# Kernel optimization log

Hardware: AMD Instinct MI355X
Metric: run time of the kernel (lower is better)

The kernel has to match this reference:

```python
import jax, jax.numpy as jnp
import numpy as np
import math
from jax import lax

K = 3  # kernel size for every layer


def _get_size(h, w, stride, ceil_mode):
    ah, aw = h - (K - 1), w - (K - 1)
    if ceil_mode:
        return math.ceil(ah / stride), math.ceil(aw / stride)
    return ah // stride, aw // stride


def _sample(h, w, stride, ceil_mode, mask_out, rng):
    """Replicates SConv2dAvg.sample: random in-stride offsets per output cell,
    plus bottom-up input mask = union of 3x3 windows of selected positions
    where the downstream mask is active."""
    ah, aw = h - (K - 1), w - (K - 1)
    oh, ow = _get_size(h, w, stride, ceil_mode)
    selh = rng.integers(0, stride, (oh, ow)).astype(np.int32)
    selw = rng.integers(0, stride, (oh, ow)).astype(np.int32)
    resth, restw = oh * stride - ah, ow * stride - aw
    if resth > 0:
        selh[-1, :] = selh[-1, :] % resth
    if restw > 0:
        selw[:, -1] = selw[:, -1] % restw
    ph = selh + (np.arange(oh) * stride)[:, None]  # conv-grid row of selected window
    pw = selw + (np.arange(ow) * stride)[None, :]
    mask_in = np.zeros((h, w), np.int32)
    ys = ph[mask_out == 1]
    xs = pw[mask_out == 1]
    for dy in range(K):
        for dx in range(K):
            mask_in[ys + dy, xs + dx] = 1
    return selh, selw, mask_in


def setup_inputs() -> dict:
    key = jax.random.key(0)
    rng = np.random.default_rng(0)
    B, H0, W0 = 64, 132, 132
    ks = jax.random.split(key, 9)
    x = jax.random.normal(ks[0], (B, 3, H0, W0), jnp.float32)

    def conv_params(kw_, kb_, cout, cin):
        bound = 1.0 / np.sqrt(cin * K * K)
        w = jax.random.uniform(kw_, (cout, cin, K, K), jnp.float32, -bound, bound)
        b = jax.random.uniform(kb_, (cout,), jnp.float32, -bound, bound)
        return w, b

    w1, b1 = conv_params(ks[1], ks[2], 200, 3)
    w2, b2 = conv_params(ks[3], ks[4], 400, 200)
    w3, b3 = conv_params(ks[5], ks[6], 800, 400)
    w4, b4 = conv_params(ks[7], ks[8], 10, 800)

    h1, wd1 = _get_size(H0, W0, 2, False)   # 65,65
    h2, wd2 = _get_size(h1, wd1, 2, False)  # 31,31
    h3, wd3 = _get_size(h2, wd2, 2, True)   # 15,15
    mask3 = np.ones((h3, wd3), np.int32)
    selh3, selw3, mask2 = _sample(h2, wd2, 2, True, mask3, rng)
    selh2, selw2, mask1 = _sample(h1, wd1, 2, False, mask2, rng)
    selh1, selw1, _ = _sample(H0, W0, 2, False, mask1, rng)

    j = jnp.asarray
    return {
        "x": x,
        "w1": w1, "b1": b1, "w2": w2, "b2": b2,
        "w3": w3, "b3": b3, "w4": w4, "b4": b4,
        "selh1": j(selh1), "selw1": j(selw1), "mask1": j(mask1),
        "selh2": j(selh2), "selw2": j(selw2), "mask2": j(mask2),
        "selh3": j(selh3), "selw3": j(selw3), "mask3": j(mask3),
    }


def _sconv_stoch(x, weight, bias, selh, selw, mask, stride):
    """Stochastic strided conv: per output cell, evaluate the 3x3 valid conv at a
    randomly selected position inside its stride x stride block; zero unmasked
    cells (they were never computed), then add bias everywhere."""
    oh, ow = selh.shape
    kh, kw = weight.shape[2], weight.shape[3]
    ph = selh + jnp.arange(oh, dtype=selh.dtype)[:, None] * stride  # (oh,ow)
    pw = selw + jnp.arange(ow, dtype=selw.dtype)[None, :] * stride
    ih = ph[:, :, None, None] + jnp.arange(kh)[None, None, :, None]  # (oh,ow,kh,kw)
    iw = pw[:, :, None, None] + jnp.arange(kw)[None, None, None, :]
    patches = x[:, :, ih, iw]  # (B, Cin, oh, ow, kh, kw)
    out = jnp.einsum('bchwij,ocij->bohw', patches, weight)
    out = jnp.where(mask[None, None] == 1, out, jnp.zeros((), out.dtype))
    return out + bias[None, :, None, None]


def reference(x, w1, b1, w2, b2, w3, b3, w4, b4,
              selh1, selw1, mask1, selh2, selw2, mask2, selh3, selw3, mask3):
    out = jax.nn.relu(_sconv_stoch(x, w1, b1, selh1, selw1, mask1, 2))
    out = jax.nn.relu(_sconv_stoch(out, w2, b2, selh2, selw2, mask2, 2))
    out = jax.nn.relu(_sconv_stoch(out, w3, b3, selh3, selw3, mask3, 2))
    out = lax.conv_general_dilated(out, w4, (1, 1), 'VALID') + b4[None, :, None, None]
    return out.reshape(out.shape[0], -1)
```

## Files before the change

kernel.cpp:

```cpp
#include <hip/hip_runtime.h>
#include <hip/hip_bf16.h>

using bf16 = __hip_bfloat16;
using short8 = __attribute__((ext_vector_type(8))) short;
using sh4 = __attribute__((ext_vector_type(4))) short;
using f32x4 = __attribute__((ext_vector_type(4))) float;

__device__ __align__(16) bf16 g_wp1[16 * 3 * 512];
__device__ __align__(16) bf16 g_wp2[63 * 32 * 512];
__device__ __align__(16) bf16 g_wp3[2 * 117 * 32 * 512];
__device__ __align__(16) bf16 g_wp4[1 * 225 * 512];

__device__ int g_list1[4225];
__device__ int g_list2[961];
__device__ int g_list3[225];
__device__ int g_cnt[3];


__global__ __launch_bounds__(256) void k_pack1(const float* __restrict__ w) {
  int el = blockIdx.x * 256 + threadIdx.x;
  if (el >= 16 * 3 * 512) return;
  int j = el & 7, lane = (el >> 3) & 63, rest = el >> 9;
  int kt = rest % 3, mt = rest / 3;
  int m = mt * 16 + (lane & 15);
  int k = kt * 32 + ((lane >> 4) * 8) + j;
  int chunk = k >> 3, c = k & 7;
  float val = 0.f;
  if (m < 200 && chunk < 9 && c < 3) val = w[((size_t)m * 3 + c) * 9 + chunk];
  g_wp1[el] = __float2bfloat16(val);
}
template <int CIN, int SUBT, int COUT, int KT>
__device__ __forceinline__ void pack_kmaj(const float* __restrict__ w,
                                          bf16* __restrict__ dst, int total) {
  int el = blockIdx.x * 256 + threadIdx.x;
  if (el >= total) return;
  int j = el & 7, lane = (el >> 3) & 63, ti = el >> 9;
  int half = ti / (KT * 32);
  int r2 = ti - half * (KT * 32);
  int kt = r2 >> 5, mtl = r2 & 31;
  int mt = half * 32 + mtl;
  int chunk = kt / SUBT, cc = kt - chunk * SUBT;
  int m = mt * 16 + (lane & 15);
  int c = cc * 32 + ((lane >> 4) * 8) + j;
  float val = 0.f;
  if (m < COUT && c < CIN) val = w[((size_t)m * CIN + c) * 9 + chunk];
  dst[el] = __float2bfloat16(val);
}
__global__ __launch_bounds__(256) void k_pack2(const float* __restrict__ w) {
  pack_kmaj<200, 7, 400, 63>(w, g_wp2, 63 * 32 * 512);
}
__global__ __launch_bounds__(256) void k_pack3(const float* __restrict__ w) {
  pack_kmaj<400, 13, 800, 117>(w, g_wp3, 2 * 117 * 32 * 512);
}
__global__ __launch_bounds__(256) void k_pack4(const float* __restrict__ w) {
  int el = blockIdx.x * 256 + threadIdx.x;
  if (el >= 225 * 512) return;
  int j = el & 7, lane = (el >> 3) & 63, rest = el >> 9;
  int kt = rest % 225;
  int chunk = kt / 25, cc = kt - chunk * 25;
  int m = lane & 15;
  int c = cc * 32 + ((lane >> 4) * 8) + j;
  float val = 0.f;
  if (m < 10 && c < 800) val = w[((size_t)m * 800 + c) * 9 + chunk];
  g_wp4[el] = __float2bfloat16(val);
}

__global__ __launch_bounds__(256) void k_compact(const int* __restrict__ m1,
                                                 const int* __restrict__ m2,
                                                 const int* __restrict__ m3) {
  const int which = blockIdx.x;
  const int* m = which == 0 ? m1 : (which == 1 ? m2 : m3);
  int* lst = which == 0 ? g_list1 : (which == 1 ? g_list2 : g_list3);
  const int n = which == 0 ? 4225 : (which == 1 ? 961 : 225);
  const int per = (n + 255) / 256;
  const int lo = threadIdx.x * per;
  const int hi = lo + per < n ? lo + per : n;
  __shared__ int cnt[256];
  __shared__ int off[256];
  int c = 0;
  for (int i = lo; i < hi; ++i) c += (m[i] != 0);
  cnt[threadIdx.x] = c;
  __syncthreads();
  if (threadIdx.x == 0) {
    int s = 0;
    for (int t = 0; t < 256; ++t) { off[t] = s; s += cnt[t]; }
    g_cnt[which] = s;
  }
  __syncthreads();
  int o = off[threadIdx.x];
  for (int i = lo; i < hi; ++i)
    if (m[i] != 0) lst[o++] = i;
}

template <int COUT>
__global__ __launch_bounds__(256) void k_fill_off(const int* __restrict__ mask,
                                                  const float* __restrict__ bias,
                                                  bf16* __restrict__ out_t) {
  constexpr int NFULL = (COUT / 32) * 32;
  constexpr int TW = COUT - NFULL;
  constexpr int TD = TW ? TW * 16 : 1;
  const int pos = blockIdx.x;
  if (mask[pos] != 0) return;
  bf16* base = out_t + (size_t)pos * 64 * COUT;
  for (int idx = threadIdx.x; idx < 64 * COUT / 8; idx += 256) {
    const int e0 = idx * 8;
    int ch0;
    if (e0 < NFULL * 64) {
      const int cc = e0 >> 11;
      const int r = e0 & 2047;
      const int lq = (r >> 7) & 3;
      ch0 = cc * 32 + lq * 8;
    } else {
      const int r = e0 - NFULL * 64;
      const int r2 = r - (r / TD) * TD;
      const int mq = (TW == 16) ? (r2 >> 7) : 0;
      ch0 = NFULL + mq * 8;
    }
    short8 s;
#pragma unroll
    for (int j = 0; j < 8; ++j) {
      float v = bias[ch0 + j];
      v = v > 0.f ? v : 0.f;
      bf16 h = __float2bfloat16(v);
      s[j] = *reinterpret_cast<short*>(&h);
    }
    *reinterpret_cast<short8*>(base + e0) = s;
  }
}

__global__ __launch_bounds__(256) void k_fill_xt(float* __restrict__ p, int n4) {
  int i = blockIdx.x * 256 + threadIdx.x;
  if (i < n4) reinterpret_cast<float4*>(p)[i] = float4{0.f, 0.f, 0.f, 0.f};
}
__global__ __launch_bounds__(256) void k_zero_out(float* __restrict__ p) {
  int i = blockIdx.x * 256 + threadIdx.x;
  if (i < 64 * 10 * 13 * 13) p[i] = 0.f;
}

__global__ __launch_bounds__(256) void k_transpose_x(const float* __restrict__ x,
                                                     bf16* __restrict__ xt) {
  int idx = blockIdx.x * 256 + threadIdx.x;
  constexpr int N = 64 * 3 * 132 * 132;
  if (idx >= N) return;
  int w = idx % 132;
  int t = idx / 132;
  int h = t % 132;
  t /= 132;
  int c = t % 3;
  int b = t / 3;
  xt[((size_t)(h * 132 + w) * 64 + b) * 8 + c] = __float2bfloat16(x[idx]);
}

template <int COUT, int MT>
__device__ __forceinline__ void epilogue_frag(f32x4 (&acc)[MT][4], int pos,
                                              int mt0, int q, int nl,
                                              const float* bias, bf16* out_t) {
  constexpr int NFULL = (COUT / 32) * 32;
  constexpr int TW = COUT - NFULL;
  bf16* cell = out_t + (size_t)pos * (COUT * 64);
#pragma unroll
  for (int ms = 0; ms < MT; ++ms) {
    const int T = mt0 + ms;
    const int mbase = T * 16 + q * 4;
    if (mbase < COUT) {
      const float4 bv = *reinterpret_cast<const float4*>(bias + mbase);
#pragma unroll
      for (int t = 0; t < 4; ++t) {
        sh4 s;
#pragma unroll
        for (int r = 0; r < 4; ++r) {
          float vv = acc[ms][t][r] + ((const float*)&bv)[r];
          vv = vv > 0.f ? vv : 0.f;
          bf16 h = __float2bfloat16(vv);
          s[r] = *reinterpret_cast<short*>(&h);
        }
        size_t el;
        if (mbase < NFULL) {
          el = ((size_t)((mbase >> 5) * 4 + t) * 64 +
                (((mbase >> 3) & 3) * 16 + nl)) * 8 + (mbase & 7);
        } else {
          el = (size_t)NFULL * 64 + t * (TW * 16) +
               ((TW == 16) ? (((mbase >> 3) & 1) * 128) : 0) + nl * 8 +
               (mbase & 7);
        }
        *reinterpret_cast<sh4*>(cell + el) = s;
      }
    }
  }
}

template <int CINW, int COUT, int WIN, int OW, int KTILES, int MT>
__device__ __forceinline__ void sconv_body_div(
    const bf16* __restrict__ in_t, const bf16* __restrict__ wp,
    const float* __restrict__ bias, const int* __restrict__ selh,
    const int* __restrict__ selw, const int* __restrict__ list, int which,
    bf16* __restrict__ out_t) {
  const int bid = blockIdx.x;
  if (bid >= g_cnt[which]) return;
  const int pos = list[bid];
  const int tid = threadIdx.x;
  const int lane = tid & 63;
  const int wv = tid >> 6;
  const int nl = lane & 15;
  const int q = lane >> 4;
  const int mt0 = blockIdx.y * (4 * MT) + wv * MT;
  f32x4 acc[MT][4] = {};
  const int y = pos / OW, xq = pos % OW;
  const int ph = selh[pos] + 2 * y;
  const int pw = selw[pos] + 2 * xq;
  const short8* ap = reinterpret_cast<const short8*>(wp);
#pragma unroll
  for (int kt = 0; kt < KTILES; ++kt) {
    int k = kt * 32 + q * 8;
    int chunk = (int)((unsigned)k / (unsigned)CINW);
    int c = k - chunk * CINW;
    if (chunk > 8) { chunk = 8; c = 0; }
    const int di = (chunk * 342) >> 10;
    const int dj = chunk - di * 3;
    const bf16* bp =
        in_t + ((size_t)((ph + di) * WIN + (pw + dj)) * 64 + nl) * CINW + c;
    short8 Bf[4];
#pragma unroll
    for (int t = 0; t < 4; ++t)
      Bf[t] = *reinterpret_cast<const short8*>(bp + (size_t)t * 16 * CINW);
    short8 Af[MT];
#pragma unroll
    for (int ms = 0; ms < MT; ++ms)
      Af[ms] = ap[((size_t)(mt0 + ms) * KTILES + kt) * 64 + lane];
#pragma unroll
    for (int ms = 0; ms < MT; ++ms)
#pragma unroll
      for (int t = 0; t < 4; ++t)
        acc[ms][t] =
            __builtin_amdgcn_mfma_f32_16x16x32_bf16(Af[ms], Bf[t], acc[ms][t], 0, 0, 0);
  }
  epilogue_frag<COUT, MT>(acc, pos, mt0, q, nl, bias, out_t);
}

template <int CIN, int SUBT, int COUT, int WIN, int OW>
__device__ __forceinline__ void sconv_body_lds(
    const bf16* __restrict__ in_t, const bf16* __restrict__ wp,
    const float* __restrict__ bias, const int* __restrict__ selh,
    const int* __restrict__ selw, const int* __restrict__ list, int which,
    int bid, int myt, bf16* __restrict__ out_t) {
  constexpr int MT = 8;
  constexpr int KTILES = 9 * SUBT;
  constexpr int NFC = CIN / 32;
  constexpr int TIN = CIN - NFC * 32;
  __shared__ __align__(16) bf16 Abuf[2][32 * 512];
  if (bid >= g_cnt[which]) return;
  const int pos = list[bid];
  const int tid = threadIdx.x;
  const int lane = tid & 63;
  const int wv = tid >> 6;
  const int nl = lane & 15;
  const int q = lane >> 4;
  const int mt0 = myt * 32 + wv * MT;
  const int y = pos / OW, xq = pos % OW;
  const int ph = selh[pos] + 2 * y;
  const int pw = selw[pos] + 2 * xq;

  auto cellp = [&](int chunk) -> const bf16* {
    const int di = (chunk * 342) >> 10;
    const int dj = chunk - di * 3;
    return in_t + (size_t)((ph + di) * WIN + (pw + dj)) * (CIN * 64);
  };
  auto stage = [&](int b, int kt) {
    const bf16* src = wp + ((size_t)kt * 32 + wv * 8) * 512;
#pragma unroll
    for (int i = 0; i < 8; ++i) {
      __builtin_amdgcn_global_load_lds(
          (const __attribute__((address_space(1))) void*)(src + (size_t)i * 512 +
                                                          (size_t)lane * 8),
          (__attribute__((address_space(3))) void*)(&Abuf[b][(wv * 8 + i) * 512]),
          16, 0, 0);
    }
  };
  auto loadB = [&](short8 (&Bf)[4], const bf16* cell, int cc) {
    if (cc < NFC) {
#pragma unroll
      for (int t = 0; t < 4; ++t)
        Bf[t] = *reinterpret_cast<const short8*>(
            cell + ((size_t)(cc * 4 + t) * 64 + lane) * 8);
    } else {
#pragma unroll
      for (int t = 0; t < 4; ++t)
        Bf[t] = *reinterpret_cast<const short8*>(
            cell + NFC * 2048 + t * (TIN * 16) +
            ((TIN == 16) ? ((q & 1) * 128) : 0) + nl * 8);
    }
  };

  f32x4 acc[MT][4] = {};
  short8 B0[4], B1[4];
  int cc = 0, chunk = 0;
  const bf16* cell = cellp(0);

  stage(0, 0);
  loadB(B0, cell, 0);

#define SSTEP(KT_, BU, BP)                                                    \
  {                                                                           \
    __builtin_amdgcn_sched_barrier(0);                                        \
    stage(((KT_) + 1) & 1, (KT_) + 1);                                        \
    int ccn = cc + 1, chn = chunk;                                            \
    const bf16* celln = cell;                                                 \
    if (ccn == SUBT) { ccn = 0; chn = chunk + 1; celln = cellp(chn); }        \
    loadB(BP, celln, ccn);                                                    \
    __builtin_amdgcn_sched_barrier(0);                                        \
    asm volatile("s_waitcnt vmcnt(12)");                                      \
    __builtin_amdgcn_sched_barrier(0);                                        \
    short8 Af[MT];                                                            \
    _Pragma("unroll") for (int ms = 0; ms < MT; ++ms)                         \
        Af[ms] = *reinterpret_cast<const short8*>(                            \
            &Abuf[(KT_) & 1][(wv * MT + ms) * 512 + lane * 8]);               \
    _Pragma("unroll") for (int ms = 0; ms < MT; ++ms)                         \
        _Pragma("unroll") for (int t = 0; t < 4; ++t)                         \
            acc[ms][t] = __builtin_amdgcn_mfma_f32_16x16x32_bf16(             \
                Af[ms], BU[t], acc[ms][t], 0, 0, 0);                          \
    cc = ccn; chunk = chn; cell = celln;                                      \
  }

  for (int kt = 0; kt + 2 <= KTILES; kt += 2) {
    SSTEP(kt, B0, B1);
    SSTEP(kt + 1, B1, B0);
  }
#undef SSTEP
  {
    __builtin_amdgcn_sched_barrier(0);
    asm volatile("s_waitcnt vmcnt(0)");
    __builtin_amdgcn_sched_barrier(0);
    short8 Af[MT];
#pragma unroll
    for (int ms = 0; ms < MT; ++ms)
      Af[ms] = *reinterpret_cast<const short8*>(
          &Abuf[(KTILES - 1) & 1][(wv * MT + ms) * 512 + lane * 8]);
#pragma unroll
    for (int ms = 0; ms < MT; ++ms)
#pragma unroll
      for (int t = 0; t < 4; ++t)
        acc[ms][t] = __builtin_amdgcn_mfma_f32_16x16x32_bf16(Af[ms], B0[t],
                                                             acc[ms][t], 0, 0, 0);
  }
  epilogue_frag<COUT, MT>(acc, pos, mt0, q, nl, bias, out_t);
}

__global__ __launch_bounds__(256) void k_sconv1(
    const bf16* __restrict__ in_t, const float* __restrict__ bias,
    const int* __restrict__ selh, const int* __restrict__ selw,
    bf16* __restrict__ out_t) {
  sconv_body_div<8, 200, 132, 65, 3, 4>(in_t, g_wp1, bias, selh, selw, g_list1, 0,
                                        out_t);
}
__global__ __launch_bounds__(256, 2) void k_sconv2(
    const bf16* __restrict__ in_t, const float* __restrict__ bias,
    const int* __restrict__ selh, const int* __restrict__ selw,
    bf16* __restrict__ out_t) {
  sconv_body_lds<200, 7, 400, 65, 31>(in_t, g_wp2, bias, selh, selw, g_list2, 1,
                                      blockIdx.x, 0, out_t);
}
__global__ __launch_bounds__(256, 2) void k_sconv3(
    const bf16* __restrict__ in_t, const float* __restrict__ bias,
    const int* __restrict__ selh, const int* __restrict__ selw,
    bf16* __restrict__ out_t) {
  const int id = blockIdx.x;
  const int xcd = id & 7;
  const int yhalf = xcd >> 2;
  const int slot = (id >> 3) * 4 + (xcd & 3);
  sconv_body_lds<400, 13, 800, 31, 15>(in_t, g_wp3 + (size_t)yhalf * 117 * 32 * 512,
                                       bias, selh, selw, g_list3, 2, slot, yhalf,
                                       out_t);
}

__global__ __launch_bounds__(256) void k_conv4m(
    const bf16* __restrict__ in_t,
    const float* __restrict__ bias,
    float* __restrict__ out) {
  const int pos = blockIdx.x;
  const int y = pos / 13, x = pos % 13;
  const int tid = threadIdx.x;
  const int lane = tid & 63;
  const int wv = tid >> 6;
  const int nl = lane & 15;
  const int q = lane >> 4;
  const int kslice = blockIdx.y * 4 + wv;
  __shared__ f32x4 Racc[4][4][64];
  f32x4 acc[4] = {};
  const short8* ap = reinterpret_cast<const short8*>(g_wp4);
  for (int kt = kslice; kt < 225; kt += 16) {
    const int chunk = kt / 25;
    const int cc = kt - chunk * 25;
    const int di = chunk / 3, dj = chunk - di * 3;
    const bf16* cell = in_t + (size_t)((y + di) * 15 + (x + dj)) * (800 * 64);
    short8 A0 = ap[(size_t)kt * 64 + lane];
    short8 Bf[4];
#pragma unroll
    for (int t = 0; t < 4; ++t)
      Bf[t] = *reinterpret_cast<const short8*>(
          cell + ((size_t)(cc * 4 + t) * 64 + lane) * 8);
#pragma unroll
    for (int t = 0; t < 4; ++t)
      acc[t] = __builtin_amdgcn_mfma_f32_16x16x32_bf16(A0, Bf[t], acc[t], 0, 0, 0);
  }
#pragma unroll
  for (int t = 0; t < 4; ++t) Racc[wv][t][lane] = acc[t];
  __syncthreads();
  if (wv == 0) {
    const int rowb = q * 4;
#pragma unroll
    for (int t = 0; t < 4; ++t) {
      f32x4 s = Racc[0][t][lane];
#pragma unroll
      for (int w2 = 1; w2 < 4; ++w2) {
        f32x4 o = Racc[w2][t][lane];
#pragma unroll
        for (int r = 0; r < 4; ++r) s[r] += o[r];
      }
      const int n = t * 16 + nl;
#pragma unroll
      for (int r = 0; r < 4; ++r) {
        const int m = rowb + r;
        if (m < 10) {
          float v = s[r] + (blockIdx.y == 0 ? bias[m] : 0.f);
          atomicAdd(&out[(((size_t)n * 10 + m) * 13 + y) * 13 + x], v);
        }
      }
    }
  }
}

extern "C" void kernel_launch(void* const* d_in, const int* in_sizes, int n_in,
                              void* d_out, int out_size, void* d_ws, size_t ws_size,
                              hipStream_t stream) {
  const float* x  = (const float*)d_in[0];
  const float* w1 = (const float*)d_in[1];
  const float* b1 = (const float*)d_in[2];
  const float* w2 = (const float*)d_in[3];
  const float* b2 = (const float*)d_in[4];
  const float* w3 = (const float*)d_in[5];
  const float* b3 = (const float*)d_in[6];
  const float* w4 = (const float*)d_in[7];
  const float* b4 = (const float*)d_in[8];
  const int* selh1 = (const int*)d_in[9];
  const int* selw1 = (const int*)d_in[10];
  const int* mask1 = (const int*)d_in[11];
  const int* selh2 = (const int*)d_in[12];
  const int* selw2 = (const int*)d_in[13];
  const int* mask2 = (const int*)d_in[14];
  const int* selh3 = (const int*)d_in[15];
  const int* selw3 = (const int*)d_in[16];
  const int* mask3 = (const int*)d_in[17];

  char* ws = (char*)d_ws;
  bf16* o1t = (bf16*)(ws);
  bf16* xt  = (bf16*)(ws + 108160000);
  bf16* o2t = (bf16*)(ws + 108160000);
  bf16* o3t = (bf16*)(ws);

  k_pack1<<<dim3((16 * 3 * 512 + 255) / 256), dim3(256), 0, stream>>>(w1);
  k_pack2<<<dim3((63 * 32 * 512 + 255) / 256), dim3(256), 0, stream>>>(w2);
  k_pack3<<<dim3((2 * 117 * 32 * 512 + 255) / 256), dim3(256), 0, stream>>>(w3);
  k_pack4<<<dim3((225 * 512 + 255) / 256), dim3(256), 0, stream>>>(w4);
  k_compact<<<dim3(3), dim3(256), 0, stream>>>(mask1, mask2, mask3);
  k_fill_xt<<<dim3((2230272 + 255) / 256), dim3(256), 0, stream>>>((float*)xt, 2230272);
  k_transpose_x<<<dim3((64 * 3 * 132 * 132 + 255) / 256), dim3(256), 0, stream>>>(x, xt);
  k_zero_out<<<dim3((64 * 10 * 13 * 13 + 255) / 256), dim3(256), 0, stream>>>(
      (float*)d_out);

  k_fill_off<200><<<dim3(4225), dim3(256), 0, stream>>>(mask1, b1, o1t);
  k_sconv1<<<dim3(4225, 1), dim3(256), 0, stream>>>(xt, b1, selh1, selw1, o1t);

  k_fill_off<400><<<dim3(961), dim3(256), 0, stream>>>(mask2, b2, o2t);
  k_sconv2<<<dim3(961, 1), dim3(256), 0, stream>>>(o1t, b2, selh2, selw2, o2t);

  k_fill_off<800><<<dim3(225), dim3(256), 0, stream>>>(mask3, b3, o3t);
  k_sconv3<<<dim3(464, 1), dim3(256), 0, stream>>>(o2t, b3, selh3, selw3, o3t);

  k_conv4m<<<dim3(13 * 13, 4), dim3(256), 0, stream>>>(o3t, b4, (float*)d_out);
}
```

Measured before the change: 468.9 us.

## Process two output positions per block to share staged weight tiles

Layers 2 and 3 now use 512-thread blocks, and each block computes two sampled output positions. Every weight A-fragment staged in LDS feeds MFMAs against both positions' activation fragments, which halves weight traffic per output. The LDS weight buffer goes from double to triple buffering, with the next stage issued after compute. Each wave now owns fewer output-channel tiles and keeps two accumulator sets, so register pressure rises and fewer blocks are launched.

```diff
diff --git a/kernel.cpp b/kernel.cpp
--- a/kernel.cpp
+++ b/kernel.cpp
@@ -238,41 +238,43 @@
 }
 
 template <int CIN, int SUBT, int COUT, int WIN, int OW>
-__device__ __forceinline__ void sconv_body_lds(
+__device__ __forceinline__ void sconv_body_pipe(
     const bf16* __restrict__ in_t, const bf16* __restrict__ wp,
     const float* __restrict__ bias, const int* __restrict__ selh,
     const int* __restrict__ selw, const int* __restrict__ list, int which,
     int bid, int myt, bf16* __restrict__ out_t) {
-  constexpr int MT = 8;
+  constexpr int MT = 4;
   constexpr int KTILES = 9 * SUBT;
   constexpr int NFC = CIN / 32;
   constexpr int TIN = CIN - NFC * 32;
-  __shared__ __align__(16) bf16 Abuf[2][32 * 512];
-  if (bid >= g_cnt[which]) return;
-  const int pos = list[bid];
+  __shared__ __align__(16) bf16 Ab[3][32 * 512];
+  const int cnt = g_cnt[which];
+  if (2 * bid >= cnt) return;
+  const int p0 = list[2 * bid];
+  const int p1 = list[2 * bid + 1 < cnt ? 2 * bid + 1 : cnt - 1];
   const int tid = threadIdx.x;
   const int lane = tid & 63;
   const int wv = tid >> 6;
   const int nl = lane & 15;
   const int q = lane >> 4;
-  const int mt0 = myt * 32 + wv * MT;
-  const int y = pos / OW, xq = pos % OW;
-  const int ph = selh[pos] + 2 * y;
-  const int pw = selw[pos] + 2 * xq;
-
-  auto cellp = [&](int chunk) -> const bf16* {
+  const int y0 = p0 / OW, x0 = p0 % OW;
+  const int y1 = p1 / OW, x1 = p1 % OW;
+  const int ph0 = selh[p0] + 2 * y0, pw0 = selw[p0] + 2 * x0;
+  const int ph1 = selh[p1] + 2 * y1, pw1 = selw[p1] + 2 * x1;
+
+  auto cellp = [&](int ph, int pw, int chunk) -> const bf16* {
     const int di = (chunk * 342) >> 10;
     const int dj = chunk - di * 3;
     return in_t + (size_t)((ph + di) * WIN + (pw + dj)) * (CIN * 64);
   };
-  auto stage = [&](int b, int kt) {
-    const bf16* src = wp + ((size_t)kt * 32 + wv * 8) * 512;
-#pragma unroll
-    for (int i = 0; i < 8; ++i) {
+  auto stage = [&](int b, int ktp) {
+    const bf16* src = wp + ((size_t)ktp * 32 + wv * 4) * 512 + lane * 8;
+#pragma unroll
+    for (int i = 0; i < 4; ++i) {
       __builtin_amdgcn_global_load_lds(
-          (const __attribute__((address_space(1))) void*)(src + (size_t)i * 512 +
-                                                          (size_t)lane * 8),
-          (__attribute__((address_space(3))) void*)(&Abuf[b][(wv * 8 + i) * 512]),
+          (const __attribute__((address_space(1))) void*)(src + (size_t)i * 512),
+          (__attribute__((address_space(3))) void*)(&Ab[b][(wv * 4 + i) * 512 +
+                                                           lane * 8]),
           16, 0, 0);
     }
   };
@@ -291,39 +293,58 @@
     }
   };
 
-  f32x4 acc[MT][4] = {};
-  short8 B0[4], B1[4];
-  int cc = 0, chunk = 0;
-  const bf16* cell = cellp(0);
+  f32x4 acc0[MT][4] = {};
+  f32x4 acc1[MT][4] = {};
+  short8 B0a[4], B0b[4], B1a[4], B1b[4];
+
+  int cc_b = 0, ch_b = 0;
+  const bf16* cellb0 = cellp(ph0, pw0, 0);
+  const bf16* cellb1 = cellp(ph1, pw1, 0);
 
   stage(0, 0);
-  loadB(B0, cell, 0);
-
-#define SSTEP(KT_, BU, BP)                                                    \
+  loadB(B0a, cellb0, 0);
+  loadB(B0b, cellb1, 0);
+  stage(1, 1);
+  if (++cc_b == SUBT) {
+    cc_b = 0;
+    ch_b = ch_b + 1 > 8 ? 8 : ch_b + 1;
+    cellb0 = cellp(ph0, pw0, ch_b);
+    cellb1 = cellp(ph1, pw1, ch_b);
+  }
+
+#define SSTEP(KT_, BUa, BUb, BPa, BPb)                                        \
   {                                                                           \
-    __builtin_amdgcn_sched_barrier(0);                                        \
-    stage(((KT_) + 1) & 1, (KT_) + 1);                                        \
-    int ccn = cc + 1, chn = chunk;                                            \
-    const bf16* celln = cell;                                                 \
-    if (ccn == SUBT) { ccn = 0; chn = chunk + 1; celln = cellp(chn); }        \
-    loadB(BP, celln, ccn);                                                    \
+    loadB(BPa, cellb0, cc_b);                                                 \
+    loadB(BPb, cellb1, cc_b);                                                 \
+    if (++cc_b == SUBT) {                                                     \
+      cc_b = 0;                                                               \
+      ch_b = ch_b + 1 > 8 ? 8 : ch_b + 1;                                     \
+      cellb0 = cellp(ph0, pw0, ch_b);                                         \
+      cellb1 = cellp(ph1, pw1, ch_b);                                         \
+    }                                                                         \
     __builtin_amdgcn_sched_barrier(0);                                        \
     asm volatile("s_waitcnt vmcnt(12)");                                      \
     __builtin_amdgcn_sched_barrier(0);                                        \
     short8 Af[MT];                                                            \
     _Pragma("unroll") for (int ms = 0; ms < MT; ++ms)                         \
         Af[ms] = *reinterpret_cast<const short8*>(                            \
-            &Abuf[(KT_) & 1][(wv * MT + ms) * 512 + lane * 8]);               \
+            &Ab[(KT_) % 3][(wv * 4 + ms) * 512 + lane * 8]);                  \
     _Pragma("unroll") for (int ms = 0; ms < MT; ++ms)                         \
-        _Pragma("unroll") for (int t = 0; t < 4; ++t)                         \
-            acc[ms][t] = __builtin_amdgcn_mfma_f32_16x16x32_bf16(             \
-                Af[ms], BU[t], acc[ms][t], 0, 0, 0);                          \
-    cc = ccn; chunk = chn; cell = celln;                                      \
+        _Pragma("unroll") for (int t = 0; t < 4; ++t) {                       \
+      acc0[ms][t] = __builtin_amdgcn_mfma_f32_16x16x32_bf16(Af[ms], BUa[t],   \
+                                                            acc0[ms][t], 0,   \
+                                                            0, 0);            \
+      acc1[ms][t] = __builtin_amdgcn_mfma_f32_16x16x32_bf16(Af[ms], BUb[t],   \
+                                                            acc1[ms][t], 0,   \
+                                                            0, 0);            \
+    }                                                                         \
+    __builtin_amdgcn_sched_barrier(0);                                        \
+    if ((KT_) + 2 < KTILES) stage(((KT_) + 2) % 3, (KT_) + 2);                \
   }
 
   for (int kt = 0; kt + 2 <= KTILES; kt += 2) {
-    SSTEP(kt, B0, B1);
-    SSTEP(kt + 1, B1, B0);
+    SSTEP(kt, B0a, B0b, B1a, B1b);
+    SSTEP(kt + 1, B1a, B1b, B0a, B0b);
   }
 #undef SSTEP
   {
@@ -334,15 +355,20 @@
 #pragma unroll
     for (int ms = 0; ms < MT; ++ms)
       Af[ms] = *reinterpret_cast<const short8*>(
-          &Abuf[(KTILES - 1) & 1][(wv * MT + ms) * 512 + lane * 8]);
+          &Ab[(KTILES - 1) % 3][(wv * 4 + ms) * 512 + lane * 8]);
 #pragma unroll
     for (int ms = 0; ms < MT; ++ms)
 #pragma unroll
-      for (int t = 0; t < 4; ++t)
-        acc[ms][t] = __builtin_amdgcn_mfma_f32_16x16x32_bf16(Af[ms], B0[t],
-                                                             acc[ms][t], 0, 0, 0);
-  }
-  epilogue_frag<COUT, MT>(acc, pos, mt0, q, nl, bias, out_t);
+      for (int t = 0; t < 4; ++t) {
+        acc0[ms][t] = __builtin_amdgcn_mfma_f32_16x16x32_bf16(Af[ms], B0a[t],
+                                                              acc0[ms][t], 0, 0, 0);
+        acc1[ms][t] = __builtin_amdgcn_mfma_f32_16x16x32_bf16(Af[ms], B0b[t],
+                                                              acc1[ms][t], 0, 0, 0);
+      }
+  }
+  const int mt0 = myt * 32 + wv * MT;
+  epilogue_frag<COUT, MT>(acc0, p0, mt0, q, nl, bias, out_t);
+  epilogue_frag<COUT, MT>(acc1, p1, mt0, q, nl, bias, out_t);
 }
 
 __global__ __launch_bounds__(256) void k_sconv1(
@@ -352,14 +378,14 @@
   sconv_body_div<8, 200, 132, 65, 3, 4>(in_t, g_wp1, bias, selh, selw, g_list1, 0,
                                         out_t);
 }
-__global__ __launch_bounds__(256, 2) void k_sconv2(
+__global__ __launch_bounds__(512, 2) void k_sconv2(
     const bf16* __restrict__ in_t, const float* __restrict__ bias,
     const int* __restrict__ selh, const int* __restrict__ selw,
     bf16* __restrict__ out_t) {
-  sconv_body_lds<200, 7, 400, 65, 31>(in_t, g_wp2, bias, selh, selw, g_list2, 1,
-                                      blockIdx.x, 0, out_t);
-}
-__global__ __launch_bounds__(256, 2) void k_sconv3(
+  sconv_body_pipe<200, 7, 400, 65, 31>(in_t, g_wp2, bias, selh, selw, g_list2, 1,
+                                       blockIdx.x, 0, out_t);
+}
+__global__ __launch_bounds__(512, 2) void k_sconv3(
     const bf16* __restrict__ in_t, const float* __restrict__ bias,
     const int* __restrict__ selh, const int* __restrict__ selw,
     bf16* __restrict__ out_t) {
@@ -367,9 +393,9 @@
   const int xcd = id & 7;
   const int yhalf = xcd >> 2;
   const int slot = (id >> 3) * 4 + (xcd & 3);
-  sconv_body_lds<400, 13, 800, 31, 15>(in_t, g_wp3 + (size_t)yhalf * 117 * 32 * 512,
-                                       bias, selh, selw, g_list3, 2, slot, yhalf,
-                                       out_t);
+  sconv_body_pipe<400, 13, 800, 31, 15>(in_t, g_wp3 + (size_t)yhalf * 117 * 32 * 512,
+                                        bias, selh, selw, g_list3, 2, slot, yhalf,
+                                        out_t);
 }
 
 __global__ __launch_bounds__(256) void k_conv4m(
@@ -471,10 +497,10 @@
   k_sconv1<<<dim3(4225, 1), dim3(256), 0, stream>>>(xt, b1, selh1, selw1, o1t);
 
   k_fill_off<400><<<dim3(961), dim3(256), 0, stream>>>(mask2, b2, o2t);
-  k_sconv2<<<dim3(961, 1), dim3(256), 0, stream>>>(o1t, b2, selh2, selw2, o2t);
+  k_sconv2<<<dim3(481, 1), dim3(512), 0, stream>>>(o1t, b2, selh2, selw2, o2t);
 
   k_fill_off<800><<<dim3(225), dim3(256), 0, stream>>>(mask3, b3, o3t);
-  k_sconv3<<<dim3(464, 1), dim3(256), 0, stream>>>(o2t, b3, selh3, selw3, o3t);
+  k_sconv3<<<dim3(232, 1), dim3(512), 0, stream>>>(o2t, b3, selh3, selw3, o3t);
 
   k_conv4m<<<dim3(13 * 13, 4), dim3(256), 0, stream>>>(o3t, b4, (float*)d_out);
 }
```

After: 468.0 us. About the same (-0.2%).
